# Kernel optimization log

Measured on AMD Instinct MI355X. Metric: run time of the kernel, lower is better.

The kernel has to match this reference:

```python
import jax, jax.numpy as jnp
import numpy as np

N, E, D = 100000, 600000, 128
BN_EPS = 1e-5


def setup_inputs() -> dict:
    key = jax.random.key(0)
    ks = jax.random.split(key, 8)
    x = jax.random.normal(ks[0], (N, D), dtype=jnp.float32)
    edge_index = jax.random.randint(ks[1], (2, E), 0, N, dtype=jnp.int64)
    # learned params: GIN eps (train_eps=True, init 0), Linear-BN-Linear MLP
    eps = jnp.zeros((), dtype=jnp.float32)
    s = 1.0 / np.sqrt(D)
    W1 = jax.random.uniform(ks[2], (D, D), jnp.float32, -s, s)
    b1 = jax.random.uniform(ks[3], (D,), jnp.float32, -s, s)
    gamma = jnp.ones((D,), jnp.float32)
    beta = jnp.zeros((D,), jnp.float32)
    W2 = jax.random.uniform(ks[4], (D, D), jnp.float32, -s, s)
    b2 = jax.random.uniform(ks[5], (D,), jnp.float32, -s, s)
    return {"x": x, "edge_index": edge_index, "eps": eps, "W1": W1, "b1": b1,
            "gamma": gamma, "beta": beta, "W2": W2, "b2": b2}


def reference(x, edge_index, eps, W1, b1, gamma, beta, W2, b2):
    src, dst = edge_index[0], edge_index[1]
    n = x.shape[0]
    # GIN aggregation: sum of neighbor features scattered to target nodes
    agg = jax.ops.segment_sum(x[src], dst, num_segments=n)  # [N, D]
    h = (1.0 + eps) * x + agg
    # MLP: Linear -> BatchNorm1d (training-mode batch stats) -> ReLU -> Linear
    h = h @ W1.T + b1
    mean = jnp.mean(h, axis=0)
    var = jnp.mean(jnp.square(h - mean), axis=0)  # biased variance, as BN uses
    h = (h - mean) * jax.lax.rsqrt(var + BN_EPS) * gamma + beta
    h = jax.nn.relu(h)
    h = h @ W2.T + b2
    # outer residual with ReLU
    return x + jax.nn.relu(h)
```

## Files before the change

### kernel.cpp

```cpp
#include <hip/hip_runtime.h>
#include <hip/hip_bf16.h>


typedef __attribute__((ext_vector_type(8))) short short8;
typedef __attribute__((ext_vector_type(4))) float f32x4;

static __device__ __forceinline__ float bf2f(unsigned short u) {
    union { unsigned int i; float f; } z; z.i = ((unsigned int)u) << 16; return z.f;
}
static __device__ __forceinline__ unsigned short f2bf(float f) {
    unsigned int u = __float_as_uint(f);
    unsigned int lsb = (u >> 16) & 1u;
    u += 0x7fffu + lsb;
    return (unsigned short)(u >> 16);
}
static __device__ __forceinline__ void atomAdd(float* p, float v) {
    __hip_atomic_fetch_add(p, v, __ATOMIC_RELAXED, __HIP_MEMORY_SCOPE_AGENT);
}
static __device__ __forceinline__ float lo16(unsigned int u) { return bf2f((unsigned short)(u & 0xffffu)); }
static __device__ __forceinline__ float hi16(unsigned int u) { return bf2f((unsigned short)(u >> 16)); }

__global__ __launch_bounds__(256) void k_detect(const unsigned short* __restrict__ gamma,
                                                const int* __restrict__ ei,
                                                int* __restrict__ flags,
                                                float* __restrict__ stats,
                                                int* __restrict__ counts, int N) {
    int idx = blockIdx.x * 256 + threadIdx.x;
    if (idx < N) counts[idx] = 0;
    if (blockIdx.x == 0) {
        int t = threadIdx.x;
        if (t < 256) stats[t] = 0.0f;
        if (t == 0) {
            flags[0] = (gamma[0] == 0x3F80u) ? 0 : 1;
            int odd = ei[1] | ei[3] | ei[5] | ei[7] | ei[9] | ei[11] | ei[13] | ei[15];
            flags[1] = (odd == 0) ? 1 : 0;
        }
    }
}

__global__ __launch_bounds__(256) void k_hist(const int* __restrict__ ei, int* __restrict__ counts,
                                              int E, const int* __restrict__ flags) {
    int e = blockIdx.x * 256 + threadIdx.x;
    if (e >= E) return;
    int dst = flags[1] ? ei[2 * E + 2 * e] : ei[E + e];
    atomicAdd(&counts[dst], 1);
}

__global__ __launch_bounds__(256) void k_scan1(const int* __restrict__ counts, int* __restrict__ partA,
                                               int N) {
    __shared__ int sd[256];
    int t = threadIdx.x, idx = blockIdx.x * 256 + t;
    sd[t] = (idx < N) ? counts[idx] : 0;
    __syncthreads();
    for (int off = 128; off > 0; off >>= 1) {
        if (t < off) sd[t] += sd[t + off];
        __syncthreads();
    }
    if (t == 0) partA[blockIdx.x] = sd[0];
}

__global__ __launch_bounds__(512) void k_scan2(const int* __restrict__ partA, int* __restrict__ partB,
                                               int NB) {
    __shared__ int sd[512];
    int t = threadIdx.x;
    sd[t] = (t < NB) ? partA[t] : 0;
    __syncthreads();
    for (int off = 1; off < 512; off <<= 1) {
        int v = (t >= off) ? sd[t - off] : 0;
        __syncthreads();
        sd[t] += v;
        __syncthreads();
    }
    if (t < NB) partB[t] = sd[t] - partA[t];
}

__global__ __launch_bounds__(256) void k_scan3(int* __restrict__ counts, int* __restrict__ rowptr,
                                               const int* __restrict__ partB, int N) {
    __shared__ int sd[256];
    int t = threadIdx.x, idx = blockIdx.x * 256 + t;
    int c = (idx < N) ? counts[idx] : 0;
    sd[t] = c;
    __syncthreads();
    for (int off = 1; off < 256; off <<= 1) {
        int v = (t >= off) ? sd[t - off] : 0;
        __syncthreads();
        sd[t] += v;
        __syncthreads();
    }
    int offB = partB[blockIdx.x];
    int excl = offB + sd[t] - c;
    if (idx < N) {
        rowptr[idx] = excl;
        counts[idx] = excl;
        if (idx == N - 1) rowptr[N] = excl + c;
    }
}

__global__ __launch_bounds__(256) void k_fill(const int* __restrict__ ei, int* __restrict__ cursor,
                                              int* __restrict__ bucket, int E,
                                              const int* __restrict__ flags) {
    int e = blockIdx.x * 256 + threadIdx.x;
    if (e >= E) return;
    int src, dst;
    if (flags[1]) { src = ei[2 * e]; dst = ei[2 * E + 2 * e]; }
    else          { src = ei[e];     dst = ei[E + e]; }
    int pos = atomicAdd(&cursor[dst], 1);
    bucket[pos] = src;
}

__global__ __launch_bounds__(256) void k_gather(const void* __restrict__ x,
                                                const void* __restrict__ eps,
                                                const int* __restrict__ rowptr,
                                                const int* __restrict__ bucket,
                                                unsigned int* __restrict__ h0, int N,
                                                const int* __restrict__ flags) {
    int wave = threadIdx.x >> 6, lane = threadIdx.x & 63;
    int n = blockIdx.x * 4 + wave;
    if (n >= N) return;
    int mode = flags[0];
    int beg = rowptr[n], end = rowptr[n + 1];
    int len = end - beg;
    float ax = 0.f, ay = 0.f;
    if (mode == 0) {
        const unsigned int* xr = (const unsigned int*)x;
        unsigned int su = xr[(size_t)n * 64 + lane];
        for (int base = 0; base < len; base += 64) {
            int rem = len - base; if (rem > 64) rem = 64;
            int idx = (lane < rem) ? bucket[beg + base + lane] : 0;
            int j = 0;
            for (; j + 8 <= rem; j += 8) {
                int s0 = __shfl(idx, j),     s1 = __shfl(idx, j + 1);
                int s2 = __shfl(idx, j + 2), s3 = __shfl(idx, j + 3);
                int s4 = __shfl(idx, j + 4), s5 = __shfl(idx, j + 5);
                int s6 = __shfl(idx, j + 6), s7 = __shfl(idx, j + 7);
                unsigned int u0 = xr[(size_t)s0 * 64 + lane];
                unsigned int u1 = xr[(size_t)s1 * 64 + lane];
                unsigned int u2 = xr[(size_t)s2 * 64 + lane];
                unsigned int u3 = xr[(size_t)s3 * 64 + lane];
                unsigned int u4 = xr[(size_t)s4 * 64 + lane];
                unsigned int u5 = xr[(size_t)s5 * 64 + lane];
                unsigned int u6 = xr[(size_t)s6 * 64 + lane];
                unsigned int u7 = xr[(size_t)s7 * 64 + lane];
                ax += ((lo16(u0) + lo16(u1)) + (lo16(u2) + lo16(u3)))
                    + ((lo16(u4) + lo16(u5)) + (lo16(u6) + lo16(u7)));
                ay += ((hi16(u0) + hi16(u1)) + (hi16(u2) + hi16(u3)))
                    + ((hi16(u4) + hi16(u5)) + (hi16(u6) + hi16(u7)));
            }
            if (j + 4 <= rem) {
                int s0 = __shfl(idx, j),     s1 = __shfl(idx, j + 1);
                int s2 = __shfl(idx, j + 2), s3 = __shfl(idx, j + 3);
                unsigned int u0 = xr[(size_t)s0 * 64 + lane];
                unsigned int u1 = xr[(size_t)s1 * 64 + lane];
                unsigned int u2 = xr[(size_t)s2 * 64 + lane];
                unsigned int u3 = xr[(size_t)s3 * 64 + lane];
                ax += (lo16(u0) + lo16(u1)) + (lo16(u2) + lo16(u3));
                ay += (hi16(u0) + hi16(u1)) + (hi16(u2) + hi16(u3));
                j += 4;
            }
            if (j + 2 <= rem) {
                int s0 = __shfl(idx, j), s1 = __shfl(idx, j + 1);
                unsigned int u0 = xr[(size_t)s0 * 64 + lane];
                unsigned int u1 = xr[(size_t)s1 * 64 + lane];
                ax += lo16(u0) + lo16(u1);
                ay += hi16(u0) + hi16(u1);
                j += 2;
            }
            if (j < rem) {
                unsigned int u = xr[(size_t)__shfl(idx, j) * 64 + lane];
                ax += lo16(u); ay += hi16(u);
            }
        }
        float s = 1.0f + bf2f(((const unsigned short*)eps)[0]);
        ax = fmaf(s, lo16(su), ax);
        ay = fmaf(s, hi16(su), ay);
    } else {
        const float2* xr = (const float2*)x;
        float2 sv = xr[(size_t)n * 64 + lane];
        for (int base = 0; base < len; base += 64) {
            int rem = len - base; if (rem > 64) rem = 64;
            int idx = (lane < rem) ? bucket[beg + base + lane] : 0;
            int j = 0;
            for (; j + 8 <= rem; j += 8) {
                int s0 = __shfl(idx, j),     s1 = __shfl(idx, j + 1);
                int s2 = __shfl(idx, j + 2), s3 = __shfl(idx, j + 3);
                int s4 = __shfl(idx, j + 4), s5 = __shfl(idx, j + 5);
                int s6 = __shfl(idx, j + 6), s7 = __shfl(idx, j + 7);
                float2 v0 = xr[(size_t)s0 * 64 + lane];
                float2 v1 = xr[(size_t)s1 * 64 + lane];
                float2 v2 = xr[(size_t)s2 * 64 + lane];
                float2 v3 = xr[(size_t)s3 * 64 + lane];
                float2 v4 = xr[(size_t)s4 * 64 + lane];
                float2 v5 = xr[(size_t)s5 * 64 + lane];
                float2 v6 = xr[(size_t)s6 * 64 + lane];
                float2 v7 = xr[(size_t)s7 * 64 + lane];
                ax += ((v0.x + v1.x) + (v2.x + v3.x)) + ((v4.x + v5.x) + (v6.x + v7.x));
                ay += ((v0.y + v1.y) + (v2.y + v3.y)) + ((v4.y + v5.y) + (v6.y + v7.y));
            }
            if (j + 4 <= rem) {
                int s0 = __shfl(idx, j),     s1 = __shfl(idx, j + 1);
                int s2 = __shfl(idx, j + 2), s3 = __shfl(idx, j + 3);
                float2 v0 = xr[(size_t)s0 * 64 + lane];
                float2 v1 = xr[(size_t)s1 * 64 + lane];
                float2 v2 = xr[(size_t)s2 * 64 + lane];
                float2 v3 = xr[(size_t)s3 * 64 + lane];
                ax += (v0.x + v1.x) + (v2.x + v3.x);
                ay += (v0.y + v1.y) + (v2.y + v3.y);
                j += 4;
            }
            for (; j < rem; ++j) {
                float2 v = xr[(size_t)__shfl(idx, j) * 64 + lane];
                ax += v.x; ay += v.y;
            }
        }
        float s = 1.0f + ((const float*)eps)[0];
        ax = fmaf(s, sv.x, ax);
        ay = fmaf(s, sv.y, ay);
    }
    h0[(size_t)n * 64 + lane] = (unsigned int)f2bf(ax) | ((unsigned int)f2bf(ay) << 16);
}

static __device__ __forceinline__ void stageW(const void* W, unsigned short* Wl,
                                              int tid, int mode) {
    for (int c = tid; c < 2048; c += 256) {
        int li = c & 15, kg = (c >> 4) & 15, t = c >> 8;
        int srcOff = (t * 16 + li) * 128 + kg * 8;
        if (mode == 0) {
            *(short8*)&Wl[c * 8] = *(const short8*)((const unsigned short*)W + srcOff);
        } else {
            const float4* wf = (const float4*)((const float*)W + srcOff);
            float4 f0 = wf[0], f1 = wf[1];
            union { short8 v; unsigned short s[8]; } u;
            u.s[0] = f2bf(f0.x); u.s[1] = f2bf(f0.y); u.s[2] = f2bf(f0.z); u.s[3] = f2bf(f0.w);
            u.s[4] = f2bf(f1.x); u.s[5] = f2bf(f1.y); u.s[6] = f2bf(f1.z); u.s[7] = f2bf(f1.w);
            *(short8*)&Wl[c * 8] = u.v;
        }
    }
}

__global__ __launch_bounds__(256, 4) void k_gemm1(const unsigned short* __restrict__ h0,
                                                  const void* __restrict__ W1,
                                                  const void* __restrict__ b1,
                                                  unsigned short* __restrict__ h1,
                                                  float* __restrict__ partials,
                                                  int N, const int* __restrict__ flags) {
    __shared__ unsigned short Wl[16384];
    __shared__ float bl[128];
    __shared__ float red_s[4][128], red_s2[4][128];
    int tid = threadIdx.x;
    int mode = flags[0];
    int lane = tid & 63, wave = tid >> 6;
    int li = lane & 15, q = lane >> 4;

    int m0 = blockIdx.x * 64 + wave * 16;
    int rowA = m0 + li; if (rowA >= N) rowA = N - 1;
    const unsigned short* ap = h0 + (size_t)rowA * 128 + q * 8;
    short8 av[4];
    av[0] = *(const short8*)(ap);
    av[1] = *(const short8*)(ap + 32);
    av[2] = *(const short8*)(ap + 64);
    av[3] = *(const short8*)(ap + 96);

    stageW(W1, Wl, tid, mode);
    if (tid < 128)
        bl[tid] = mode ? ((const float*)b1)[tid] : bf2f(((const unsigned short*)b1)[tid]);
    __syncthreads();

    f32x4 acc[8] = {};
#pragma unroll
    for (int c4 = 0; c4 < 4; ++c4) {
#pragma unroll
        for (int t = 0; t < 8; ++t) {
            short8 bfrag = *(const short8*)&Wl[(t * 256 + (c4 * 4 + q) * 16 + li) * 8];
            acc[t] = __builtin_amdgcn_mfma_f32_16x16x32_bf16(av[c4], bfrag, acc[t], 0, 0, 0);
        }
    }

    float s_acc[8] = {0.f, 0.f, 0.f, 0.f, 0.f, 0.f, 0.f, 0.f};
    float s2_acc[8] = {0.f, 0.f, 0.f, 0.f, 0.f, 0.f, 0.f, 0.f};
    bool full = (m0 + 16 <= N);
    if (full) {
        unsigned short* hp = h1 + (size_t)(m0 + q * 4) * 128 + li;
#pragma unroll
        for (int t = 0; t < 8; ++t) {
            float bb = bl[t * 16 + li];
#pragma unroll
            for (int r = 0; r < 4; ++r) {
                float v = acc[t][r] + bb;
                hp[(size_t)r * 128 + t * 16] = f2bf(v);
                s_acc[t] += v; s2_acc[t] += v * v;
            }
        }
    } else if (m0 < N) {
#pragma unroll
        for (int t = 0; t < 8; ++t) {
            int col = t * 16 + li;
            float bb = bl[col];
#pragma unroll
            for (int r = 0; r < 4; ++r) {
                int row = m0 + q * 4 + r;
                if (row < N) {
                    float v = acc[t][r] + bb;
                    h1[(size_t)row * 128 + col] = f2bf(v);
                    s_acc[t] += v; s2_acc[t] += v * v;
                }
            }
        }
    }
#pragma unroll
    for (int t = 0; t < 8; ++t) {
        float s = s_acc[t], s2 = s2_acc[t];
        s  += __shfl_xor(s, 16);  s  += __shfl_xor(s, 32);
        s2 += __shfl_xor(s2, 16); s2 += __shfl_xor(s2, 32);
        if (lane < 16) { red_s[wave][t * 16 + li] = s; red_s2[wave][t * 16 + li] = s2; }
    }
    __syncthreads();
    float pv;
    if (tid < 128) {
        pv = red_s[0][tid] + red_s[1][tid] + red_s[2][tid] + red_s[3][tid];
    } else {
        int c = tid - 128;
        pv = red_s2[0][c] + red_s2[1][c] + red_s2[2][c] + red_s2[3][c];
    }
    partials[(size_t)blockIdx.x * 256 + tid] = pv;
}

__global__ __launch_bounds__(256) void k_reduce(const float* __restrict__ partials,
                                                float* __restrict__ stats, int nb) {
    int t = threadIdx.x;
    float acc = 0.f;
    for (int b = blockIdx.x; b < nb; b += 64)
        acc += partials[(size_t)b * 256 + t];
    atomAdd(&stats[t], acc);
}

__global__ __launch_bounds__(256, 4) void k_gemm2(const unsigned short* __restrict__ h1,
                                                  const void* __restrict__ W2,
                                                  const void* __restrict__ b2,
                                                  const float* __restrict__ stats,
                                                  const void* __restrict__ gamma,
                                                  const void* __restrict__ beta,
                                                  const void* __restrict__ x,
                                                  void* __restrict__ out, int N, float invN,
                                                  const int* __restrict__ flags) {
    __shared__ unsigned short Wl[16384];
    __shared__ float bl[128], al[128], cl[128];
    int tid = threadIdx.x;
    int mode = flags[0];
    int lane = tid & 63, wave = tid >> 6;
    int li = lane & 15, q = lane >> 4;

    int m0 = blockIdx.x * 64 + wave * 16;
    int rowA = m0 + li; if (rowA >= N) rowA = N - 1;
    const unsigned short* ap = h1 + (size_t)rowA * 128 + q * 8;
    short8 hv[4];
    hv[0] = *(const short8*)(ap);
    hv[1] = *(const short8*)(ap + 32);
    hv[2] = *(const short8*)(ap + 64);
    hv[3] = *(const short8*)(ap + 96);

    stageW(W2, Wl, tid, mode);
    if (tid < 128) {
        bl[tid] = mode ? ((const float*)b2)[tid] : bf2f(((const unsigned short*)b2)[tid]);
        float mean = stats[tid] * invN;
        float var = stats[128 + tid] * invN - mean * mean;
        float g  = mode ? ((const float*)gamma)[tid] : bf2f(((const unsigned short*)gamma)[tid]);
        float bt = mode ? ((const float*)beta)[tid]  : bf2f(((const unsigned short*)beta)[tid]);
        float a = g * rsqrtf(var + 1e-5f);
        al[tid] = a;
        cl[tid] = bt - mean * a;
    }
    __syncthreads();

    short8 au[4];
#pragma unroll
    for (int c4 = 0; c4 < 4; ++c4) {
        int k0 = c4 * 32 + q * 8;
        union { short8 v; unsigned short s[8]; } hu; hu.v = hv[c4];
        float4 sa = *(const float4*)&al[k0];
        float4 sb = *(const float4*)&al[k0 + 4];
        float4 ca = *(const float4*)&cl[k0];
        float4 cb = *(const float4*)&cl[k0 + 4];
        union { short8 v; unsigned short s[8]; } uu;
        uu.s[0] = f2bf(fmaxf(fmaf(bf2f(hu.s[0]), sa.x, ca.x), 0.f));
        uu.s[1] = f2bf(fmaxf(fmaf(bf2f(hu.s[1]), sa.y, ca.y), 0.f));
        uu.s[2] = f2bf(fmaxf(fmaf(bf2f(hu.s[2]), sa.z, ca.z), 0.f));
        uu.s[3] = f2bf(fmaxf(fmaf(bf2f(hu.s[3]), sa.w, ca.w), 0.f));
        uu.s[4] = f2bf(fmaxf(fmaf(bf2f(hu.s[4]), sb.x, cb.x), 0.f));
        uu.s[5] = f2bf(fmaxf(fmaf(bf2f(hu.s[5]), sb.y, cb.y), 0.f));
        uu.s[6] = f2bf(fmaxf(fmaf(bf2f(hu.s[6]), sb.z, cb.z), 0.f));
        uu.s[7] = f2bf(fmaxf(fmaf(bf2f(hu.s[7]), sb.w, cb.w), 0.f));
        au[c4] = uu.v;
    }

    bool full = (m0 + 16 <= N);
    float xv[32];
    if (full) {
        if (mode == 0) {
            const unsigned short* xp = (const unsigned short*)x + (size_t)(m0 + q * 4) * 128 + li;
#pragma unroll
            for (int t = 0; t < 8; ++t)
#pragma unroll
                for (int r = 0; r < 4; ++r)
                    xv[t * 4 + r] = bf2f(xp[(size_t)r * 128 + t * 16]);
        } else {
            const float* xp = (const float*)x + (size_t)(m0 + q * 4) * 128 + li;
#pragma unroll
            for (int t = 0; t < 8; ++t)
#pragma unroll
                for (int r = 0; r < 4; ++r)
                    xv[t * 4 + r] = xp[(size_t)r * 128 + t * 16];
        }
    }

    f32x4 acc[8] = {};
#pragma unroll
    for (int c4 = 0; c4 < 4; ++c4) {
#pragma unroll
        for (int t = 0; t < 8; ++t) {
            short8 bfrag = *(const short8*)&Wl[(t * 256 + (c4 * 4 + q) * 16 + li) * 8];
            acc[t] = __builtin_amdgcn_mfma_f32_16x16x32_bf16(au[c4], bfrag, acc[t], 0, 0, 0);
        }
    }

    if (full) {
        if (mode == 0) {
            unsigned short* op = (unsigned short*)out + (size_t)(m0 + q * 4) * 128 + li;
#pragma unroll
            for (int t = 0; t < 8; ++t) {
                float bb = bl[t * 16 + li];
#pragma unroll
                for (int r = 0; r < 4; ++r)
                    op[(size_t)r * 128 + t * 16] =
                        f2bf(xv[t * 4 + r] + fmaxf(acc[t][r] + bb, 0.f));
            }
        } else {
            float* op = (float*)out + (size_t)(m0 + q * 4) * 128 + li;
#pragma unroll
            for (int t = 0; t < 8; ++t) {
                float bb = bl[t * 16 + li];
#pragma unroll
                for (int r = 0; r < 4; ++r)
                    op[(size_t)r * 128 + t * 16] =
                        xv[t * 4 + r] + fmaxf(acc[t][r] + bb, 0.f);
            }
        }
    } else if (m0 < N) {
#pragma unroll
        for (int t = 0; t < 8; ++t) {
            int col = t * 16 + li;
            float bb = bl[col];
#pragma unroll
            for (int r = 0; r < 4; ++r) {
                int row = m0 + q * 4 + r;
                if (row < N) {
                    size_t idx = (size_t)row * 128 + col;
                    float v = fmaxf(acc[t][r] + bb, 0.f);
                    if (mode == 0) {
                        float xvs = bf2f(((const unsigned short*)x)[idx]);
                        ((unsigned short*)out)[idx] = f2bf(xvs + v);
                    } else {
                        float xvs = ((const float*)x)[idx];
                        ((float*)out)[idx] = xvs + v;
                    }
                }
            }
        }
    }
}

extern "C" void kernel_launch(void* const* d_in, const int* in_sizes, int n_in,
                              void* d_out, int out_size, void* d_ws, size_t ws_size,
                              hipStream_t stream) {
    const void* x     = d_in[0];
    const int*  ei    = (const int*)d_in[1];
    const void* eps   = d_in[2];
    const void* W1    = d_in[3];
    const void* b1    = d_in[4];
    const void* gamma = d_in[5];
    const void* beta  = d_in[6];
    const void* W2    = d_in[7];
    const void* b2    = d_in[8];

    int N = in_sizes[0] / 128;
    int E = in_sizes[1] / 2;

    unsigned short* h0 = (unsigned short*)d_ws;
    unsigned short* h1 = h0 + (size_t)N * 128;
    int* counts = (int*)(h1 + (size_t)N * 128);
    int* rowptr = counts + N;
    int* bucket = rowptr + N + 1;
    int* partA  = bucket + E;
    int* partB  = partA + 512;
    float* stats = (float*)(partB + 512);
    int*   flags = (int*)(stats + 256);
    float* tail  = (float*)(flags + 16);

    int NB = (N + 255) / 256;
    int EB = (E + 255) / 256;
    int mb = (N + 63) / 64;

    size_t partials_elems = (size_t)mb * 256;
    size_t dead_elems = (size_t)N + (size_t)(N + 1) + (size_t)E;
    float* partials = (partials_elems <= dead_elems) ? (float*)counts : tail;

    k_detect<<<NB, 256, 0, stream>>>((const unsigned short*)gamma, ei, flags, stats, counts, N);
    k_hist<<<EB, 256, 0, stream>>>(ei, counts, E, flags);
    k_scan1<<<NB, 256, 0, stream>>>(counts, partA, N);
    k_scan2<<<1, 512, 0, stream>>>(partA, partB, NB);
    k_scan3<<<NB, 256, 0, stream>>>(counts, rowptr, partB, N);
    k_fill<<<EB, 256, 0, stream>>>(ei, counts, bucket, E, flags);

    k_gather<<<(N + 3) / 4, 256, 0, stream>>>(x, eps, rowptr, bucket,
                                              (unsigned int*)h0, N, flags);

    k_gemm1<<<mb, 256, 0, stream>>>(h0, W1, b1, h1, partials, N, flags);
    k_reduce<<<64, 256, 0, stream>>>(partials, stats, mb);
    k_gemm2<<<mb, 256, 0, stream>>>(h1, W2, b2, stats, gamma, beta, x, d_out, N,
                                    1.0f / (float)N, flags);
}
```

Baseline: 291.9 us.

## Fuse neighbor gather-aggregation into GEMM1 via swizzled LDS A-tile

Removes the separate gather kernel. Each wave of GEMM1 now aggregates neighbor features for its 16 rows directly into a swizzled shared-memory bf16 tile, prefetching the next node's bucket indices, then runs the MFMA from LDS. This drops the h0 round trip through global memory and one kernel launch. In exchange GEMM1 uses more LDS and has launch bounds lowered from 4 to 3 blocks, so fewer waves are in flight to hide the irregular gather latency. The BN partial sums now reuse the W LDS buffer and the unused h0 workspace.

```diff
diff --git a/kernel.cpp b/kernel.cpp
--- a/kernel.cpp
+++ b/kernel.cpp
@@ -108,117 +108,6 @@
     bucket[pos] = src;
 }
 
-__global__ __launch_bounds__(256) void k_gather(const void* __restrict__ x,
-                                                const void* __restrict__ eps,
-                                                const int* __restrict__ rowptr,
-                                                const int* __restrict__ bucket,
-                                                unsigned int* __restrict__ h0, int N,
-                                                const int* __restrict__ flags) {
-    int wave = threadIdx.x >> 6, lane = threadIdx.x & 63;
-    int n = blockIdx.x * 4 + wave;
-    if (n >= N) return;
-    int mode = flags[0];
-    int beg = rowptr[n], end = rowptr[n + 1];
-    int len = end - beg;
-    float ax = 0.f, ay = 0.f;
-    if (mode == 0) {
-        const unsigned int* xr = (const unsigned int*)x;
-        unsigned int su = xr[(size_t)n * 64 + lane];
-        for (int base = 0; base < len; base += 64) {
-            int rem = len - base; if (rem > 64) rem = 64;
-            int idx = (lane < rem) ? bucket[beg + base + lane] : 0;
-            int j = 0;
-            for (; j + 8 <= rem; j += 8) {
-                int s0 = __shfl(idx, j),     s1 = __shfl(idx, j + 1);
-                int s2 = __shfl(idx, j + 2), s3 = __shfl(idx, j + 3);
-                int s4 = __shfl(idx, j + 4), s5 = __shfl(idx, j + 5);
-                int s6 = __shfl(idx, j + 6), s7 = __shfl(idx, j + 7);
-                unsigned int u0 = xr[(size_t)s0 * 64 + lane];
-                unsigned int u1 = xr[(size_t)s1 * 64 + lane];
-                unsigned int u2 = xr[(size_t)s2 * 64 + lane];
-                unsigned int u3 = xr[(size_t)s3 * 64 + lane];
-                unsigned int u4 = xr[(size_t)s4 * 64 + lane];
-                unsigned int u5 = xr[(size_t)s5 * 64 + lane];
-                unsigned int u6 = xr[(size_t)s6 * 64 + lane];
-                unsigned int u7 = xr[(size_t)s7 * 64 + lane];
-                ax += ((lo16(u0) + lo16(u1)) + (lo16(u2) + lo16(u3)))
-                    + ((lo16(u4) + lo16(u5)) + (lo16(u6) + lo16(u7)));
-                ay += ((hi16(u0) + hi16(u1)) + (hi16(u2) + hi16(u3)))
-                    + ((hi16(u4) + hi16(u5)) + (hi16(u6) + hi16(u7)));
-            }
-            if (j + 4 <= rem) {
-                int s0 = __shfl(idx, j),     s1 = __shfl(idx, j + 1);
-                int s2 = __shfl(idx, j + 2), s3 = __shfl(idx, j + 3);
-                unsigned int u0 = xr[(size_t)s0 * 64 + lane];
-                unsigned int u1 = xr[(size_t)s1 * 64 + lane];
-                unsigned int u2 = xr[(size_t)s2 * 64 + lane];
-                unsigned int u3 = xr[(size_t)s3 * 64 + lane];
-                ax += (lo16(u0) + lo16(u1)) + (lo16(u2) + lo16(u3));
-                ay += (hi16(u0) + hi16(u1)) + (hi16(u2) + hi16(u3));
-                j += 4;
-            }
-            if (j + 2 <= rem) {
-                int s0 = __shfl(idx, j), s1 = __shfl(idx, j + 1);
-                unsigned int u0 = xr[(size_t)s0 * 64 + lane];
-                unsigned int u1 = xr[(size_t)s1 * 64 + lane];
-                ax += lo16(u0) + lo16(u1);
-                ay += hi16(u0) + hi16(u1);
-                j += 2;
-            }
-            if (j < rem) {
-                unsigned int u = xr[(size_t)__shfl(idx, j) * 64 + lane];
-                ax += lo16(u); ay += hi16(u);
-            }
-        }
-        float s = 1.0f + bf2f(((const unsigned short*)eps)[0]);
-        ax = fmaf(s, lo16(su), ax);
-        ay = fmaf(s, hi16(su), ay);
-    } else {
-        const float2* xr = (const float2*)x;
-        float2 sv = xr[(size_t)n * 64 + lane];
-        for (int base = 0; base < len; base += 64) {
-            int rem = len - base; if (rem > 64) rem = 64;
-            int idx = (lane < rem) ? bucket[beg + base + lane] : 0;
-            int j = 0;
-            for (; j + 8 <= rem; j += 8) {
-                int s0 = __shfl(idx, j),     s1 = __shfl(idx, j + 1);
-                int s2 = __shfl(idx, j + 2), s3 = __shfl(idx, j + 3);
-                int s4 = __shfl(idx, j + 4), s5 = __shfl(idx, j + 5);
-                int s6 = __shfl(idx, j + 6), s7 = __shfl(idx, j + 7);
-                float2 v0 = xr[(size_t)s0 * 64 + lane];
-                float2 v1 = xr[(size_t)s1 * 64 + lane];
-                float2 v2 = xr[(size_t)s2 * 64 + lane];
-                float2 v3 = xr[(size_t)s3 * 64 + lane];
-                float2 v4 = xr[(size_t)s4 * 64 + lane];
-                float2 v5 = xr[(size_t)s5 * 64 + lane];
-                float2 v6 = xr[(size_t)s6 * 64 + lane];
-                float2 v7 = xr[(size_t)s7 * 64 + lane];
-                ax += ((v0.x + v1.x) + (v2.x + v3.x)) + ((v4.x + v5.x) + (v6.x + v7.x));
-                ay += ((v0.y + v1.y) + (v2.y + v3.y)) + ((v4.y + v5.y) + (v6.y + v7.y));
-            }
-            if (j + 4 <= rem) {
-                int s0 = __shfl(idx, j),     s1 = __shfl(idx, j + 1);
-                int s2 = __shfl(idx, j + 2), s3 = __shfl(idx, j + 3);
-                float2 v0 = xr[(size_t)s0 * 64 + lane];
-                float2 v1 = xr[(size_t)s1 * 64 + lane];
-                float2 v2 = xr[(size_t)s2 * 64 + lane];
-                float2 v3 = xr[(size_t)s3 * 64 + lane];
-                ax += (v0.x + v1.x) + (v2.x + v3.x);
-                ay += (v0.y + v1.y) + (v2.y + v3.y);
-                j += 4;
-            }
-            for (; j < rem; ++j) {
-                float2 v = xr[(size_t)__shfl(idx, j) * 64 + lane];
-                ax += v.x; ay += v.y;
-            }
-        }
-        float s = 1.0f + ((const float*)eps)[0];
-        ax = fmaf(s, sv.x, ax);
-        ay = fmaf(s, sv.y, ay);
-    }
-    h0[(size_t)n * 64 + lane] = (unsigned int)f2bf(ax) | ((unsigned int)f2bf(ay) << 16);
-}
-
 static __device__ __forceinline__ void stageW(const void* W, unsigned short* Wl,
                                               int tid, int mode) {
     for (int c = tid; c < 2048; c += 256) {
@@ -237,44 +126,183 @@
     }
 }
 
-__global__ __launch_bounds__(256, 4) void k_gemm1(const unsigned short* __restrict__ h0,
+__global__ __launch_bounds__(256, 3) void k_gemm1(const void* __restrict__ x,
+                                                  const void* __restrict__ eps,
+                                                  const int* __restrict__ rowptr,
+                                                  const int* __restrict__ bucket,
                                                   const void* __restrict__ W1,
                                                   const void* __restrict__ b1,
                                                   unsigned short* __restrict__ h1,
                                                   float* __restrict__ partials,
                                                   int N, const int* __restrict__ flags) {
     __shared__ unsigned short Wl[16384];
+    __shared__ unsigned int At[4096];
     __shared__ float bl[128];
-    __shared__ float red_s[4][128], red_s2[4][128];
     int tid = threadIdx.x;
     int mode = flags[0];
     int lane = tid & 63, wave = tid >> 6;
     int li = lane & 15, q = lane >> 4;
-
-    int m0 = blockIdx.x * 64 + wave * 16;
-    int rowA = m0 + li; if (rowA >= N) rowA = N - 1;
-    const unsigned short* ap = h0 + (size_t)rowA * 128 + q * 8;
-    short8 av[4];
-    av[0] = *(const short8*)(ap);
-    av[1] = *(const short8*)(ap + 32);
-    av[2] = *(const short8*)(ap + 64);
-    av[3] = *(const short8*)(ap + 96);
+    int r0 = blockIdx.x * 64 + wave * 16;
+
+    int rl = lane < 16 ? lane : 16;
+    int rq = r0 + rl; if (rq > N) rq = N;
+    int rpv = rowptr[rq];
 
     stageW(W1, Wl, tid, mode);
     if (tid < 128)
         bl[tid] = mode ? ((const float*)b1)[tid] : bf2f(((const unsigned short*)b1)[tid]);
-    __syncthreads();
-
+
+    if (mode == 0) {
+        const unsigned int* xr = (const unsigned int*)x;
+        float s = 1.0f + bf2f(((const unsigned short*)eps)[0]);
+        int begN = __shfl(rpv, 0), endN = __shfl(rpv, 1);
+        int idxN = 0;
+        { int l0 = endN - begN; if (l0 > 64) l0 = 64;
+          if (lane < l0) idxN = bucket[begN + lane]; }
+        for (int node = 0; node < 16; ++node) {
+            int row = r0 + node;
+            int rowc = row < N ? row : N - 1;
+            int beg = begN, end = endN, idx = idxN;
+            if (node < 15) {
+                begN = __shfl(rpv, node + 1); endN = __shfl(rpv, node + 2);
+                int ln = endN - begN; if (ln > 64) ln = 64;
+                idxN = (lane < ln) ? bucket[begN + lane] : 0;
+            }
+            unsigned int su = xr[(size_t)rowc * 64 + lane];
+            int len = end - beg;
+            float ax = 0.f, ay = 0.f;
+            for (int base = 0; base < len; base += 64) {
+                int rem = len - base; if (rem > 64) rem = 64;
+                int idw = (base == 0) ? idx
+                        : ((lane < rem) ? bucket[beg + base + lane] : 0);
+                int j = 0;
+                for (; j + 8 <= rem; j += 8) {
+                    int s0 = __shfl(idw, j),     s1 = __shfl(idw, j + 1);
+                    int s2 = __shfl(idw, j + 2), s3 = __shfl(idw, j + 3);
+                    int s4 = __shfl(idw, j + 4), s5 = __shfl(idw, j + 5);
+                    int s6 = __shfl(idw, j + 6), s7 = __shfl(idw, j + 7);
+                    unsigned int u0 = xr[(size_t)s0 * 64 + lane];
+                    unsigned int u1 = xr[(size_t)s1 * 64 + lane];
+                    unsigned int u2 = xr[(size_t)s2 * 64 + lane];
+                    unsigned int u3 = xr[(size_t)s3 * 64 + lane];
+                    unsigned int u4 = xr[(size_t)s4 * 64 + lane];
+                    unsigned int u5 = xr[(size_t)s5 * 64 + lane];
+                    unsigned int u6 = xr[(size_t)s6 * 64 + lane];
+                    unsigned int u7 = xr[(size_t)s7 * 64 + lane];
+                    ax += ((lo16(u0) + lo16(u1)) + (lo16(u2) + lo16(u3)))
+                        + ((lo16(u4) + lo16(u5)) + (lo16(u6) + lo16(u7)));
+                    ay += ((hi16(u0) + hi16(u1)) + (hi16(u2) + hi16(u3)))
+                        + ((hi16(u4) + hi16(u5)) + (hi16(u6) + hi16(u7)));
+                }
+                if (j + 4 <= rem) {
+                    int s0 = __shfl(idw, j),     s1 = __shfl(idw, j + 1);
+                    int s2 = __shfl(idw, j + 2), s3 = __shfl(idw, j + 3);
+                    unsigned int u0 = xr[(size_t)s0 * 64 + lane];
+                    unsigned int u1 = xr[(size_t)s1 * 64 + lane];
+                    unsigned int u2 = xr[(size_t)s2 * 64 + lane];
+                    unsigned int u3 = xr[(size_t)s3 * 64 + lane];
+                    ax += (lo16(u0) + lo16(u1)) + (lo16(u2) + lo16(u3));
+                    ay += (hi16(u0) + hi16(u1)) + (hi16(u2) + hi16(u3));
+                    j += 4;
+                }
+                if (j + 2 <= rem) {
+                    int s0 = __shfl(idw, j), s1 = __shfl(idw, j + 1);
+                    unsigned int u0 = xr[(size_t)s0 * 64 + lane];
+                    unsigned int u1 = xr[(size_t)s1 * 64 + lane];
+                    ax += lo16(u0) + lo16(u1);
+                    ay += hi16(u0) + hi16(u1);
+                    j += 2;
+                }
+                if (j < rem) {
+                    unsigned int u = xr[(size_t)__shfl(idw, j) * 64 + lane];
+                    ax += lo16(u); ay += hi16(u);
+                }
+            }
+            ax = fmaf(s, lo16(su), ax);
+            ay = fmaf(s, hi16(su), ay);
+            int lr = wave * 16 + node;
+            At[lr * 64 + (((lane >> 2) ^ (lr & 15)) << 2) + (lane & 3)] =
+                (unsigned int)f2bf(ax) | ((unsigned int)f2bf(ay) << 16);
+        }
+    } else {
+        const float2* xr = (const float2*)x;
+        float s = 1.0f + ((const float*)eps)[0];
+        int begN = __shfl(rpv, 0), endN = __shfl(rpv, 1);
+        int idxN = 0;
+        { int l0 = endN - begN; if (l0 > 64) l0 = 64;
+          if (lane < l0) idxN = bucket[begN + lane]; }
+        for (int node = 0; node < 16; ++node) {
+            int row = r0 + node;
+            int rowc = row < N ? row : N - 1;
+            int beg = begN, end = endN, idx = idxN;
+            if (node < 15) {
+                begN = __shfl(rpv, node + 1); endN = __shfl(rpv, node + 2);
+                int ln = endN - begN; if (ln > 64) ln = 64;
+                idxN = (lane < ln) ? bucket[begN + lane] : 0;
+            }
+            float2 sv = xr[(size_t)rowc * 64 + lane];
+            int len = end - beg;
+            float ax = 0.f, ay = 0.f;
+            for (int base = 0; base < len; base += 64) {
+                int rem = len - base; if (rem > 64) rem = 64;
+                int idw = (base == 0) ? idx
+                        : ((lane < rem) ? bucket[beg + base + lane] : 0);
+                int j = 0;
+                for (; j + 8 <= rem; j += 8) {
+                    int s0 = __shfl(idw, j),     s1 = __shfl(idw, j + 1);
+                    int s2 = __shfl(idw, j + 2), s3 = __shfl(idw, j + 3);
+                    int s4 = __shfl(idw, j + 4), s5 = __shfl(idw, j + 5);
+                    int s6 = __shfl(idw, j + 6), s7 = __shfl(idw, j + 7);
+                    float2 v0 = xr[(size_t)s0 * 64 + lane];
+                    float2 v1 = xr[(size_t)s1 * 64 + lane];
+                    float2 v2 = xr[(size_t)s2 * 64 + lane];
+                    float2 v3 = xr[(size_t)s3 * 64 + lane];
+                    float2 v4 = xr[(size_t)s4 * 64 + lane];
+                    float2 v5 = xr[(size_t)s5 * 64 + lane];
+                    float2 v6 = xr[(size_t)s6 * 64 + lane];
+                    float2 v7 = xr[(size_t)s7 * 64 + lane];
+                    ax += ((v0.x + v1.x) + (v2.x + v3.x)) + ((v4.x + v5.x) + (v6.x + v7.x));
+                    ay += ((v0.y + v1.y) + (v2.y + v3.y)) + ((v4.y + v5.y) + (v6.y + v7.y));
+                }
+                if (j + 4 <= rem) {
+                    int s0 = __shfl(idw, j),     s1 = __shfl(idw, j + 1);
+                    int s2 = __shfl(idw, j + 2), s3 = __shfl(idw, j + 3);
+                    float2 v0 = xr[(size_t)s0 * 64 + lane];
+                    float2 v1 = xr[(size_t)s1 * 64 + lane];
+                    float2 v2 = xr[(size_t)s2 * 64 + lane];
+                    float2 v3 = xr[(size_t)s3 * 64 + lane];
+                    ax += (v0.x + v1.x) + (v2.x + v3.x);
+                    ay += (v0.y + v1.y) + (v2.y + v3.y);
+                    j += 4;
+                }
+                for (; j < rem; ++j) {
+                    float2 v = xr[(size_t)__shfl(idw, j) * 64 + lane];
+                    ax += v.x; ay += v.y;
+                }
+            }
+            ax = fmaf(s, sv.x, ax);
+            ay = fmaf(s, sv.y, ay);
+            int lr = wave * 16 + node;
+            At[lr * 64 + (((lane >> 2) ^ (lr & 15)) << 2) + (lane & 3)] =
+                (unsigned int)f2bf(ax) | ((unsigned int)f2bf(ay) << 16);
+        }
+    }
+    __syncthreads();
+
+    int lrb = wave * 16 + li;
     f32x4 acc[8] = {};
 #pragma unroll
     for (int c4 = 0; c4 < 4; ++c4) {
+        int k = c4 * 4 + q;
+        short8 av = *(const short8*)&At[lrb * 64 + ((k ^ li) << 2)];
 #pragma unroll
         for (int t = 0; t < 8; ++t) {
-            short8 bfrag = *(const short8*)&Wl[(t * 256 + (c4 * 4 + q) * 16 + li) * 8];
-            acc[t] = __builtin_amdgcn_mfma_f32_16x16x32_bf16(av[c4], bfrag, acc[t], 0, 0, 0);
-        }
-    }
-
+            short8 bfrag = *(const short8*)&Wl[(t * 256 + k * 16 + li) * 8];
+            acc[t] = __builtin_amdgcn_mfma_f32_16x16x32_bf16(av, bfrag, acc[t], 0, 0, 0);
+        }
+    }
+
+    int m0 = r0;
     float s_acc[8] = {0.f, 0.f, 0.f, 0.f, 0.f, 0.f, 0.f, 0.f};
     float s2_acc[8] = {0.f, 0.f, 0.f, 0.f, 0.f, 0.f, 0.f, 0.f};
     bool full = (m0 + 16 <= N);
@@ -306,20 +334,25 @@
             }
         }
     }
+    __syncthreads();
+    float* redu = (float*)Wl;
 #pragma unroll
     for (int t = 0; t < 8; ++t) {
         float s = s_acc[t], s2 = s2_acc[t];
         s  += __shfl_xor(s, 16);  s  += __shfl_xor(s, 32);
         s2 += __shfl_xor(s2, 16); s2 += __shfl_xor(s2, 32);
-        if (lane < 16) { red_s[wave][t * 16 + li] = s; red_s2[wave][t * 16 + li] = s2; }
+        if (lane < 16) {
+            redu[wave * 128 + t * 16 + li] = s;
+            redu[512 + wave * 128 + t * 16 + li] = s2;
+        }
     }
     __syncthreads();
     float pv;
     if (tid < 128) {
-        pv = red_s[0][tid] + red_s[1][tid] + red_s[2][tid] + red_s[3][tid];
+        pv = redu[tid] + redu[128 + tid] + redu[256 + tid] + redu[384 + tid];
     } else {
-        int c = tid - 128;
-        pv = red_s2[0][c] + red_s2[1][c] + red_s2[2][c] + red_s2[3][c];
+        int c = tid - 128 + 512;
+        pv = redu[c] + redu[128 + c] + redu[256 + c] + redu[384 + c];
     }
     partials[(size_t)blockIdx.x * 256 + tid] = pv;
 }
@@ -493,15 +526,12 @@
     int* partB  = partA + 512;
     float* stats = (float*)(partB + 512);
     int*   flags = (int*)(stats + 256);
-    float* tail  = (float*)(flags + 16);
 
     int NB = (N + 255) / 256;
     int EB = (E + 255) / 256;
     int mb = (N + 63) / 64;
 
-    size_t partials_elems = (size_t)mb * 256;
-    size_t dead_elems = (size_t)N + (size_t)(N + 1) + (size_t)E;
-    float* partials = (partials_elems <= dead_elems) ? (float*)counts : tail;
+    float* partials = (float*)h0;
 
     k_detect<<<NB, 256, 0, stream>>>((const unsigned short*)gamma, ei, flags, stats, counts, N);
     k_hist<<<EB, 256, 0, stream>>>(ei, counts, E, flags);
@@ -510,10 +540,8 @@
     k_scan3<<<NB, 256, 0, stream>>>(counts, rowptr, partB, N);
     k_fill<<<EB, 256, 0, stream>>>(ei, counts, bucket, E, flags);
 
-    k_gather<<<(N + 3) / 4, 256, 0, stream>>>(x, eps, rowptr, bucket,
-                                              (unsigned int*)h0, N, flags);
-
-    k_gemm1<<<mb, 256, 0, stream>>>(h0, W1, b1, h1, partials, N, flags);
+    k_gemm1<<<mb, 256, 0, stream>>>(x, eps, rowptr, bucket, W1, b1, h1,
+                                    partials, N, flags);
     k_reduce<<<64, 256, 0, stream>>>(partials, stats, mb);
     k_gemm2<<<mb, 256, 0, stream>>>(h1, W2, b2, stats, gamma, beta, x, d_out, N,
                                     1.0f / (float)N, flags);
```

Result: slower. 312.6 us (+7.1%).
